# Performance work log

Hardware: AMD Instinct MI355X
Metric: run time of the kernel (lower is better)

The kernel has to match this reference:

```python
import jax, jax.numpy as jnp
import numpy as np

N_NODES = 100000
N_EDGES = 600000
D_FEAT = 128
OUT_DIM = 128


def setup_inputs() -> dict:
    key = jax.random.key(0)
    k_x, k_r, k_c, k_v, k_w = jax.random.split(key, 5)
    x = jax.random.normal(k_x, (N_NODES, D_FEAT), dtype=jnp.float32)
    adj_rows = jax.random.randint(k_r, (N_EDGES,), 0, N_NODES, dtype=jnp.int64 if jax.config.jax_enable_x64 else jnp.int32).astype(jnp.int32)
    adj_cols = jax.random.randint(k_c, (N_EDGES,), 0, N_NODES, dtype=jnp.int32)
    adj_vals = jax.random.uniform(k_v, (N_EDGES,), dtype=jnp.float32)
    # Xavier-uniform init for W of shape [2*d, out]
    fan_in, fan_out = 2 * D_FEAT, OUT_DIM
    bound = float(np.sqrt(6.0 / (fan_in + fan_out)))
    W = jax.random.uniform(k_w, (2 * D_FEAT, OUT_DIM), minval=-bound, maxval=bound, dtype=jnp.float32)
    return {"x": x, "adj_rows": adj_rows, "adj_cols": adj_cols, "adj_vals": adj_vals, "W": W}


def reference(x, adj_rows, adj_cols, adj_vals, W):
    # h = A @ x  via COO SpMM: gather neighbor features, scale, segment-sum by row
    msgs = adj_vals[:, None] * x[adj_cols]            # [E, d]
    h = jax.ops.segment_sum(msgs, adj_rows, num_segments=N_NODES)  # [N, d]
    # concat([h, x]) @ W == h @ W[:d] + x @ W[d:]  (avoids materializing concat)
    out = h @ W[:D_FEAT] + x @ W[D_FEAT:]             # [N, out]
    return jax.nn.relu(out)
```

## Files before the change

### kernel.cpp

```cpp
#include <hip/hip_runtime.h>
#include <hip/hip_bf16.h>

constexpr int N_NODES = 100000;
constexpr int N_EDGES = 600000;
constexpr int D = 128;
constexpr int CAP = 32;
constexpr int NRANGE = 8;
constexpr int ROWS_PER_RANGE = N_NODES / NRANGE;

constexpr size_t X16_OFF  = 0;
constexpr size_t WP_OFF   = 25600000;
constexpr size_t CNT_OFF  = 25665536;
constexpr size_t BINS_OFF = 26065536;

typedef __attribute__((ext_vector_type(8))) short short8;
typedef __attribute__((ext_vector_type(4))) float float4v;

__device__ inline unsigned short f2bf(float f) {
    union { float f; unsigned int u; } v; v.f = f;
    unsigned int u = v.u + 0x7fffu + ((v.u >> 16) & 1u);
    return (unsigned short)(u >> 16);
}
__device__ inline float bf2f(unsigned int lo16) {
    union { unsigned int u; float f; } v; v.u = lo16 << 16;
    return v.f;
}

__global__ __launch_bounds__(256) void prep_kernel(
    const float* __restrict__ x, uint4* __restrict__ x16,
    const float* __restrict__ W, unsigned short* __restrict__ Wp,
    const int* __restrict__ rows, const int* __restrict__ cols,
    const float* __restrict__ vals,
    int* __restrict__ cnt, int2* __restrict__ bins)
{
    const int tid = blockIdx.x * 256 + threadIdx.x;
    const int T   = gridDim.x * 256;

    for (int idx = tid; idx < 8 * 8 * 64 * 8; idx += T) {
        int j    = idx & 7;
        int lane = (idx >> 3) & 63;
        int jt   = (idx >> 9) & 7;
        int s    = idx >> 12;
        int k = s * 32 + (lane >> 4) * 8 + j;
        int n = jt * 16 + (lane & 15);
        Wp[idx] = f2bf(W[k * 128 + n]);
    }

    for (int g = tid; g < N_NODES * D / 8; g += T) {
        const float4* xp = reinterpret_cast<const float4*>(x + (size_t)g * 8);
        float4 a = xp[0], c = xp[1];
        uint4 o;
        o.x = (unsigned int)f2bf(a.x) | ((unsigned int)f2bf(a.y) << 16);
        o.y = (unsigned int)f2bf(a.z) | ((unsigned int)f2bf(a.w) << 16);
        o.z = (unsigned int)f2bf(c.x) | ((unsigned int)f2bf(c.y) << 16);
        o.w = (unsigned int)f2bf(c.z) | ((unsigned int)f2bf(c.w) << 16);
        x16[g] = o;
    }

    {
        const int p   = blockIdx.x & 7;
        const int rlo = p * ROWS_PER_RANGE;
        const int rhi = rlo + ROWS_PER_RANGE;
        const int sb  = (int)(blockIdx.x >> 3);
        const int nsl = (int)(gridDim.x >> 3);
        const int elen = (N_EDGES + nsl - 1) / nsl;
        const int e0 = sb * elen;
        int e1 = e0 + elen; if (e1 > N_EDGES) e1 = N_EDGES;
        for (int e = e0 + threadIdx.x; e < e1; e += 256) {
            int r = rows[e];
            if (r >= rlo && r < rhi) {
                int pos = atomicAdd(&cnt[r], 1);
                if (pos < CAP)
                    bins[(size_t)r * CAP + pos] =
                        make_int2(cols[e], __float_as_int(vals[e]));
            }
        }
    }
}

__global__ __launch_bounds__(256) void fused_agg_gemm_kernel(
    const uint4* __restrict__ x16v,
    const unsigned short* __restrict__ x16s,
    const int* __restrict__ cnt,
    const int2* __restrict__ bins,
    const unsigned short* __restrict__ Wp,
    float* __restrict__ out)
{
    __shared__ uint4 lds4[256];

    const int tid  = threadIdx.x;
    const int wave = tid >> 6;
    const int lane = tid & 63;
    const int row0 = blockIdx.x * 16;

    {
        const int G  = wave * 4 + (lane >> 4);
        const int gl = lane & 15;
        const int n  = row0 + G;

        const int4* b2 = reinterpret_cast<const int4*>(bins + (size_t)n * CAP);
        const int  d   = cnt[n];
        const int4 c0 = b2[0], c1 = b2[1], c2 = b2[2], c3 = b2[3];
        const int dend = d > CAP ? CAP : d;

        int col0 = c0.x; col0 = col0 < 0 ? 0 : col0;
        col0 = col0 >= N_NODES ? N_NODES - 1 : col0;
        const int cc1 = (1 < dend) ? c0.z : col0;
        const int cc2 = (2 < dend) ? c1.x : col0;
        const int cc3 = (3 < dend) ? c1.z : col0;
        const int cc4 = (4 < dend) ? c2.x : col0;
        const int cc5 = (5 < dend) ? c2.z : col0;
        const int cc6 = (6 < dend) ? c3.x : col0;
        const int cc7 = (7 < dend) ? c3.z : col0;
        const float v0 = (0 < dend) ? __int_as_float(c0.y) : 0.f;
        const float v1 = (1 < dend) ? __int_as_float(c0.w) : 0.f;
        const float v2 = (2 < dend) ? __int_as_float(c1.y) : 0.f;
        const float v3 = (3 < dend) ? __int_as_float(c1.w) : 0.f;
        const float v4 = (4 < dend) ? __int_as_float(c2.y) : 0.f;
        const float v5 = (5 < dend) ? __int_as_float(c2.w) : 0.f;
        const float v6 = (6 < dend) ? __int_as_float(c3.y) : 0.f;
        const float v7 = (7 < dend) ? __int_as_float(c3.w) : 0.f;

        const uint4 p0 = x16v[(size_t)col0 * 16 + gl];
        const uint4 p1 = x16v[(size_t)cc1  * 16 + gl];
        const uint4 p2 = x16v[(size_t)cc2  * 16 + gl];
        const uint4 p3 = x16v[(size_t)cc3  * 16 + gl];
        const uint4 p4 = x16v[(size_t)cc4  * 16 + gl];
        const uint4 p5 = x16v[(size_t)cc5  * 16 + gl];
        const uint4 p6 = x16v[(size_t)cc6  * 16 + gl];
        const uint4 p7 = x16v[(size_t)cc7  * 16 + gl];

        float a0, a1, a2, a3, a4, a5, a6, a7;
        a0  = v0 * bf2f(p0.x & 0xffffu) + v1 * bf2f(p1.x & 0xffffu)
            + v2 * bf2f(p2.x & 0xffffu) + v3 * bf2f(p3.x & 0xffffu)
            + v4 * bf2f(p4.x & 0xffffu) + v5 * bf2f(p5.x & 0xffffu)
            + v6 * bf2f(p6.x & 0xffffu) + v7 * bf2f(p7.x & 0xffffu);
        a1  = v0 * bf2f(p0.x >> 16)     + v1 * bf2f(p1.x >> 16)
            + v2 * bf2f(p2.x >> 16)     + v3 * bf2f(p3.x >> 16)
            + v4 * bf2f(p4.x >> 16)     + v5 * bf2f(p5.x >> 16)
            + v6 * bf2f(p6.x >> 16)     + v7 * bf2f(p7.x >> 16);
        a2  = v0 * bf2f(p0.y & 0xffffu) + v1 * bf2f(p1.y & 0xffffu)
            + v2 * bf2f(p2.y & 0xffffu) + v3 * bf2f(p3.y & 0xffffu)
            + v4 * bf2f(p4.y & 0xffffu) + v5 * bf2f(p5.y & 0xffffu)
            + v6 * bf2f(p6.y & 0xffffu) + v7 * bf2f(p7.y & 0xffffu);
        a3  = v0 * bf2f(p0.y >> 16)     + v1 * bf2f(p1.y >> 16)
            + v2 * bf2f(p2.y >> 16)     + v3 * bf2f(p3.y >> 16)
            + v4 * bf2f(p4.y >> 16)     + v5 * bf2f(p5.y >> 16)
            + v6 * bf2f(p6.y >> 16)     + v7 * bf2f(p7.y >> 16);
        a4  = v0 * bf2f(p0.z & 0xffffu) + v1 * bf2f(p1.z & 0xffffu)
            + v2 * bf2f(p2.z & 0xffffu) + v3 * bf2f(p3.z & 0xffffu)
            + v4 * bf2f(p4.z & 0xffffu) + v5 * bf2f(p5.z & 0xffffu)
            + v6 * bf2f(p6.z & 0xffffu) + v7 * bf2f(p7.z & 0xffffu);
        a5  = v0 * bf2f(p0.z >> 16)     + v1 * bf2f(p1.z >> 16)
            + v2 * bf2f(p2.z >> 16)     + v3 * bf2f(p3.z >> 16)
            + v4 * bf2f(p4.z >> 16)     + v5 * bf2f(p5.z >> 16)
            + v6 * bf2f(p6.z >> 16)     + v7 * bf2f(p7.z >> 16);
        a6  = v0 * bf2f(p0.w & 0xffffu) + v1 * bf2f(p1.w & 0xffffu)
            + v2 * bf2f(p2.w & 0xffffu) + v3 * bf2f(p3.w & 0xffffu)
            + v4 * bf2f(p4.w & 0xffffu) + v5 * bf2f(p5.w & 0xffffu)
            + v6 * bf2f(p6.w & 0xffffu) + v7 * bf2f(p7.w & 0xffffu);
        a7  = v0 * bf2f(p0.w >> 16)     + v1 * bf2f(p1.w >> 16)
            + v2 * bf2f(p2.w >> 16)     + v3 * bf2f(p3.w >> 16)
            + v4 * bf2f(p4.w >> 16)     + v5 * bf2f(p5.w >> 16)
            + v6 * bf2f(p6.w >> 16)     + v7 * bf2f(p7.w >> 16);

        if (dend > 8) {
            const int2* bp = bins + (size_t)n * CAP;
            for (int i = 8; i < dend; i += 4) {
                const int i1 = (i + 1 < dend) ? i + 1 : dend - 1;
                const int i2 = (i + 2 < dend) ? i + 2 : dend - 1;
                const int i3 = (i + 3 < dend) ? i + 3 : dend - 1;
                int2 e0 = bp[i];
                int2 e1 = bp[i1];
                int2 e2 = bp[i2];
                int2 e3 = bp[i3];
                uint4 q0 = x16v[(size_t)e0.x * 16 + gl];
                uint4 q1 = x16v[(size_t)e1.x * 16 + gl];
                uint4 q2 = x16v[(size_t)e2.x * 16 + gl];
                uint4 q3 = x16v[(size_t)e3.x * 16 + gl];
                float w0 = __int_as_float(e0.y);
                float w1 = (i + 1 < dend) ? __int_as_float(e1.y) : 0.f;
                float w2 = (i + 2 < dend) ? __int_as_float(e2.y) : 0.f;
                float w3 = (i + 3 < dend) ? __int_as_float(e3.y) : 0.f;
                a0 += w0 * bf2f(q0.x & 0xffffu) + w1 * bf2f(q1.x & 0xffffu)
                    + w2 * bf2f(q2.x & 0xffffu) + w3 * bf2f(q3.x & 0xffffu);
                a1 += w0 * bf2f(q0.x >> 16)     + w1 * bf2f(q1.x >> 16)
                    + w2 * bf2f(q2.x >> 16)     + w3 * bf2f(q3.x >> 16);
                a2 += w0 * bf2f(q0.y & 0xffffu) + w1 * bf2f(q1.y & 0xffffu)
                    + w2 * bf2f(q2.y & 0xffffu) + w3 * bf2f(q3.y & 0xffffu);
                a3 += w0 * bf2f(q0.y >> 16)     + w1 * bf2f(q1.y >> 16)
                    + w2 * bf2f(q2.y >> 16)     + w3 * bf2f(q3.y >> 16);
                a4 += w0 * bf2f(q0.z & 0xffffu) + w1 * bf2f(q1.z & 0xffffu)
                    + w2 * bf2f(q2.z & 0xffffu) + w3 * bf2f(q3.z & 0xffffu);
                a5 += w0 * bf2f(q0.z >> 16)     + w1 * bf2f(q1.z >> 16)
                    + w2 * bf2f(q2.z >> 16)     + w3 * bf2f(q3.z >> 16);
                a6 += w0 * bf2f(q0.w & 0xffffu) + w1 * bf2f(q1.w & 0xffffu)
                    + w2 * bf2f(q2.w & 0xffffu) + w3 * bf2f(q3.w & 0xffffu);
                a7 += w0 * bf2f(q0.w >> 16)     + w1 * bf2f(q1.w >> 16)
                    + w2 * bf2f(q2.w >> 16)     + w3 * bf2f(q3.w >> 16);
            }
        }

        uint4 o;
        o.x = (unsigned int)f2bf(a0) | ((unsigned int)f2bf(a1) << 16);
        o.y = (unsigned int)f2bf(a2) | ((unsigned int)f2bf(a3) << 16);
        o.z = (unsigned int)f2bf(a4) | ((unsigned int)f2bf(a5) << 16);
        o.w = (unsigned int)f2bf(a6) | ((unsigned int)f2bf(a7) << 16);
        lds4[(gl >> 2) * 64 + G * 4 + (gl & 3)] = o;
    }
    __syncthreads();

    const int m    = lane & 15;
    const int quad = lane >> 4;
    const int jt0  = wave * 2;
    const int jt1  = jt0 + 1;

    const unsigned short* xrow = x16s + (size_t)(row0 + m) * D + quad * 8;

    float4v acc0 = (float4v){0.f, 0.f, 0.f, 0.f};
    float4v acc1 = (float4v){0.f, 0.f, 0.f, 0.f};

    #pragma unroll
    for (int s = 0; s < 8; s++) {
        short8 a;
        if (s < 4)
            a = *reinterpret_cast<const short8*>(&lds4[s * 64 + m * 4 + quad]);
        else
            a = *reinterpret_cast<const short8*>(xrow + (s - 4) * 32);
        short8 b0 = *reinterpret_cast<const short8*>(
            Wp + ((size_t)((s * 8 + jt0) * 64 + lane)) * 8);
        short8 b1 = *reinterpret_cast<const short8*>(
            Wp + ((size_t)((s * 8 + jt1) * 64 + lane)) * 8);
        acc0 = __builtin_amdgcn_mfma_f32_16x16x32_bf16(a, b0, acc0, 0, 0, 0);
        acc1 = __builtin_amdgcn_mfma_f32_16x16x32_bf16(a, b1, acc1, 0, 0, 0);
    }

    #pragma unroll
    for (int reg = 0; reg < 4; reg++) {
        const int r = row0 + quad * 4 + reg;
        float* orow = out + (size_t)r * D;
        orow[jt0 * 16 + m] = fmaxf(acc0[reg], 0.f);
        orow[jt1 * 16 + m] = fmaxf(acc1[reg], 0.f);
    }
}

extern "C" void kernel_launch(void* const* d_in, const int* in_sizes, int n_in,
                              void* d_out, int out_size, void* d_ws, size_t ws_size,
                              hipStream_t stream)
{
    const float* x    = (const float*)d_in[0];
    const int*   rows = (const int*)  d_in[1];
    const int*   cols = (const int*)  d_in[2];
    const float* vals = (const float*)d_in[3];
    const float* W    = (const float*)d_in[4];
    float* out = (float*)d_out;

    char* ws = (char*)d_ws;
    uint4*          x16v = (uint4*)         (ws + X16_OFF);
    unsigned short* x16s = (unsigned short*)(ws + X16_OFF);
    unsigned short* Wp   = (unsigned short*)(ws + WP_OFF);
    int*            cnt  = (int*)           (ws + CNT_OFF);
    int2*           bins = (int2*)          (ws + BINS_OFF);

    hipMemsetAsync(cnt, 0, N_NODES * sizeof(int), stream);
    prep_kernel<<<2048, 256, 0, stream>>>(x, x16v, W, Wp, rows, cols, vals, cnt, bins);
    fused_agg_gemm_kernel<<<N_NODES / 16, 256, 0, stream>>>(
        x16v, x16s, cnt, bins, Wp, out);
}
```

Measured before the change: 189.4 us.

## Split prep into cast and bin kernels, use nontemporal loads/stores

Splits the combined prep kernel into a cast kernel and a separate binning kernel. The binning kernel processes every edge once with a grid-stride loop, replacing the old scheme in which eight row-range block groups each scanned their own edge slice. Nontemporal loads and stores are added for streaming data (x, edge arrays, bins, output) so they bypass or deprioritise the cache. This adds an extra kernel launch, and the bin writes become less localised by row range, so atomics and bin stores may scatter across all rows.

```diff
diff --git a/kernel.cpp b/kernel.cpp
--- a/kernel.cpp
+++ b/kernel.cpp
@@ -5,8 +5,6 @@
 constexpr int N_EDGES = 600000;
 constexpr int D = 128;
 constexpr int CAP = 32;
-constexpr int NRANGE = 8;
-constexpr int ROWS_PER_RANGE = N_NODES / NRANGE;
 
 constexpr size_t X16_OFF  = 0;
 constexpr size_t WP_OFF   = 25600000;
@@ -15,6 +13,8 @@
 
 typedef __attribute__((ext_vector_type(8))) short short8;
 typedef __attribute__((ext_vector_type(4))) float float4v;
+typedef __attribute__((ext_vector_type(4))) float float4e;
+typedef __attribute__((ext_vector_type(4))) int   int4e;
 
 __device__ inline unsigned short f2bf(float f) {
     union { float f; unsigned int u; } v; v.f = f;
@@ -26,12 +26,9 @@
     return v.f;
 }
 
-__global__ __launch_bounds__(256) void prep_kernel(
+__global__ __launch_bounds__(256) void prep_cast_kernel(
     const float* __restrict__ x, uint4* __restrict__ x16,
-    const float* __restrict__ W, unsigned short* __restrict__ Wp,
-    const int* __restrict__ rows, const int* __restrict__ cols,
-    const float* __restrict__ vals,
-    int* __restrict__ cnt, int2* __restrict__ bins)
+    const float* __restrict__ W, unsigned short* __restrict__ Wp)
 {
     const int tid = blockIdx.x * 256 + threadIdx.x;
     const int T   = gridDim.x * 256;
@@ -47,8 +44,9 @@
     }
 
     for (int g = tid; g < N_NODES * D / 8; g += T) {
-        const float4* xp = reinterpret_cast<const float4*>(x + (size_t)g * 8);
-        float4 a = xp[0], c = xp[1];
+        const float4e* xp = reinterpret_cast<const float4e*>(x + (size_t)g * 8);
+        float4e a = __builtin_nontemporal_load(xp);
+        float4e c = __builtin_nontemporal_load(xp + 1);
         uint4 o;
         o.x = (unsigned int)f2bf(a.x) | ((unsigned int)f2bf(a.y) << 16);
         o.y = (unsigned int)f2bf(a.z) | ((unsigned int)f2bf(a.w) << 16);
@@ -56,25 +54,23 @@
         o.w = (unsigned int)f2bf(c.z) | ((unsigned int)f2bf(c.w) << 16);
         x16[g] = o;
     }
-
-    {
-        const int p   = blockIdx.x & 7;
-        const int rlo = p * ROWS_PER_RANGE;
-        const int rhi = rlo + ROWS_PER_RANGE;
-        const int sb  = (int)(blockIdx.x >> 3);
-        const int nsl = (int)(gridDim.x >> 3);
-        const int elen = (N_EDGES + nsl - 1) / nsl;
-        const int e0 = sb * elen;
-        int e1 = e0 + elen; if (e1 > N_EDGES) e1 = N_EDGES;
-        for (int e = e0 + threadIdx.x; e < e1; e += 256) {
-            int r = rows[e];
-            if (r >= rlo && r < rhi) {
-                int pos = atomicAdd(&cnt[r], 1);
-                if (pos < CAP)
-                    bins[(size_t)r * CAP + pos] =
-                        make_int2(cols[e], __float_as_int(vals[e]));
-            }
-        }
+}
+
+__global__ __launch_bounds__(256) void prep_bin_kernel(
+    const int* __restrict__ rows, const int* __restrict__ cols,
+    const float* __restrict__ vals,
+    int* __restrict__ cnt, int2* __restrict__ bins)
+{
+    const int tid = blockIdx.x * 256 + threadIdx.x;
+    const int T   = gridDim.x * 256;
+
+    for (int e = tid; e < N_EDGES; e += T) {
+        int r = __builtin_nontemporal_load(rows + e);
+        int c = __builtin_nontemporal_load(cols + e);
+        float v = __builtin_nontemporal_load(vals + e);
+        int pos = atomicAdd(&cnt[r], 1);
+        if (pos < CAP)
+            bins[(size_t)r * CAP + pos] = make_int2(c, __float_as_int(v));
     }
 }
 
@@ -98,9 +94,12 @@
         const int gl = lane & 15;
         const int n  = row0 + G;
 
-        const int4* b2 = reinterpret_cast<const int4*>(bins + (size_t)n * CAP);
+        const int4e* b2 = reinterpret_cast<const int4e*>(bins + (size_t)n * CAP);
         const int  d   = cnt[n];
-        const int4 c0 = b2[0], c1 = b2[1], c2 = b2[2], c3 = b2[3];
+        const int4e c0 = __builtin_nontemporal_load(b2 + 0);
+        const int4e c1 = __builtin_nontemporal_load(b2 + 1);
+        const int4e c2 = __builtin_nontemporal_load(b2 + 2);
+        const int4e c3 = __builtin_nontemporal_load(b2 + 3);
         const int dend = d > CAP ? CAP : d;
 
         int col0 = c0.x; col0 = col0 < 0 ? 0 : col0;
@@ -239,8 +238,8 @@
     for (int reg = 0; reg < 4; reg++) {
         const int r = row0 + quad * 4 + reg;
         float* orow = out + (size_t)r * D;
-        orow[jt0 * 16 + m] = fmaxf(acc0[reg], 0.f);
-        orow[jt1 * 16 + m] = fmaxf(acc1[reg], 0.f);
+        __builtin_nontemporal_store(fmaxf(acc0[reg], 0.f), orow + jt0 * 16 + m);
+        __builtin_nontemporal_store(fmaxf(acc1[reg], 0.f), orow + jt1 * 16 + m);
     }
 }
 
@@ -263,7 +262,8 @@
     int2*           bins = (int2*)          (ws + BINS_OFF);
 
     hipMemsetAsync(cnt, 0, N_NODES * sizeof(int), stream);
-    prep_kernel<<<2048, 256, 0, stream>>>(x, x16v, W, Wp, rows, cols, vals, cnt, bins);
+    prep_cast_kernel<<<2048, 256, 0, stream>>>(x, x16v, W, Wp);
+    prep_bin_kernel<<<2048, 256, 0, stream>>>(rows, cols, vals, cnt, bins);
     fused_agg_gemm_kernel<<<N_NODES / 16, 256, 0, stream>>>(
         x16v, x16s, cnt, bins, Wp, out);
 }
```

After: 197.3 us. +4.1%, slower.
